# Performance work log

Measured on AMD Instinct MI355X. Metric: run time of the kernel, lower is better.

The kernel has to match this reference:

```python
import jax, jax.numpy as jnp
from jax import lax
import numpy as np

BETA = 0.25
K = 64   # num_embeddings
D = 64   # embedding_dim (must equal K per module's view(-1, D))
HID = 128
RES = 64
N_RES = 2


def _conv(x, w, b=None, stride=1, pad=0):
    y = lax.conv_general_dilated(x, w, (stride, stride), [(pad, pad), (pad, pad)],
                                 dimension_numbers=('NCHW', 'OIHW', 'NCHW'))
    if b is not None:
        y = y + b[None, :, None, None]
    return y


def _deconv(x, w, b, stride, pad):
    # torch ConvTranspose2d weight is (Cin, Cout, k, k); emulate via lhs-dilated conv with flipped kernel
    k = w.shape[2]
    p = k - 1 - pad
    w2 = jnp.transpose(w[:, :, ::-1, ::-1], (1, 0, 2, 3))  # -> (Cout, Cin, k, k)
    y = lax.conv_general_dilated(x, w2, (1, 1), [(p, p), (p, p)], lhs_dilation=(stride, stride),
                                 dimension_numbers=('NCHW', 'OIHW', 'NCHW'))
    return y + b[None, :, None, None]


def _res_block(x, w1, w2):
    # [Residual_Layer]*N_RES shares ONE set of weights; in-place ReLU means skip adds relu(x)
    for _ in range(N_RES):
        r = jax.nn.relu(x)
        h = _conv(r, w1, pad=1)
        h = jax.nn.relu(h)
        h = _conv(h, w2)
        x = r + h
    return jax.nn.relu(x)


def setup_inputs() -> dict:
    key = jax.random.key(0)
    ks = jax.random.split(key, 16)
    f32 = jnp.float32
    s = 0.05
    inp = {
        'x': jax.random.normal(ks[0], (32, 1, 256, 256), f32),
        # encoder
        'enc_c1_w': jax.random.normal(ks[1], (HID // 2, 1, 4, 4), f32) * s,
        'enc_c1_b': jnp.zeros((HID // 2,), f32),
        'enc_c2_w': jax.random.normal(ks[2], (HID, HID // 2, 4, 4), f32) * s,
        'enc_c2_b': jnp.zeros((HID,), f32),
        'enc_c3_w': jax.random.normal(ks[3], (HID, HID, 3, 3), f32) * s,
        'enc_c3_b': jnp.zeros((HID,), f32),
        'enc_r1_w': jax.random.normal(ks[4], (RES, HID, 3, 3), f32) * s,
        'enc_r2_w': jax.random.normal(ks[5], (HID, RES, 1, 1), f32) * s,
        # pre-VQ 1x1 conv: hidden -> K channels
        'vqc_w': jax.random.normal(ks[6], (K, HID, 1, 1), f32) * s,
        'vqc_b': jnp.zeros((K,), f32),
        # codebook, uniform(-1/K, 1/K)
        'emb': jax.random.uniform(ks[7], (K, D), f32, -1.0 / K, 1.0 / K),
        # decoder (ConvTranspose2d weights are (Cin, Cout, k, k))
        'dec_c1_w': jax.random.normal(ks[8], (D, HID, 3, 3), f32) * s,
        'dec_c1_b': jnp.zeros((HID,), f32),
        'dec_r1_w': jax.random.normal(ks[9], (RES, HID, 3, 3), f32) * s,
        'dec_r2_w': jax.random.normal(ks[10], (HID, RES, 1, 1), f32) * s,
        'dec_c2_w': jax.random.normal(ks[11], (HID, HID // 2, 4, 4), f32) * s,
        'dec_c2_b': jnp.zeros((HID // 2,), f32),
        'dec_c3_w': jax.random.normal(ks[12], (HID // 2, 1, 4, 4), f32) * s,
        'dec_c3_b': jnp.zeros((1,), f32),
    }
    return inp


def reference(x, enc_c1_w, enc_c1_b, enc_c2_w, enc_c2_b, enc_c3_w, enc_c3_b,
              enc_r1_w, enc_r2_w, vqc_w, vqc_b, emb,
              dec_c1_w, dec_c1_b, dec_r1_w, dec_r2_w, dec_c2_w, dec_c2_b, dec_c3_w, dec_c3_b):
    # ---- encoder ----
    h = jax.nn.relu(_conv(x, enc_c1_w, enc_c1_b, stride=2, pad=1))
    h = jax.nn.relu(_conv(h, enc_c2_w, enc_c2_b, stride=2, pad=1))
    h = _conv(h, enc_c3_w, enc_c3_b, pad=1)
    h = _res_block(h, enc_r1_w, enc_r2_w)
    z = _conv(h, vqc_w, vqc_b)  # (B, K, 64, 64)

    # ---- VQ ----
    zt = jnp.transpose(z, (0, 2, 3, 1))            # (B, H, W, D)
    flat = zt.reshape(-1, D)                        # (N, D)
    dist = (jnp.sum(flat ** 2, axis=1, keepdims=True)
            + jnp.sum(emb ** 2, axis=1)
            - 2.0 * flat @ emb.T)                   # (N, K)
    idx = jnp.argmin(dist, axis=1)                  # (N,)
    onehot = jax.nn.one_hot(idx, K, dtype=flat.dtype)
    q = (onehot @ emb).reshape(zt.shape)
    commitment = jnp.mean((lax.stop_gradient(q) - zt) ** 2)
    embedding_l = jnp.mean((q - lax.stop_gradient(zt)) ** 2)
    loss = commitment * BETA + embedding_l
    q_st = zt + lax.stop_gradient(q - zt)           # straight-through
    mean_enc = jnp.mean(onehot, axis=0)
    perplexity = jnp.exp(-jnp.sum(mean_enc * jnp.log(mean_enc + 1e-10)))
    qn = jnp.transpose(q_st, (0, 3, 1, 2))          # (B, D, 64, 64)

    # ---- decoder ----
    d = _deconv(qn, dec_c1_w, dec_c1_b, 1, 1)
    d = _res_block(d, dec_r1_w, dec_r2_w)
    d = jax.nn.relu(_deconv(d, dec_c2_w, dec_c2_b, 2, 1))
    x_re = jnp.tanh(_deconv(d, dec_c3_w, dec_c3_b, 2, 1))
    return (loss, x_re, perplexity, qn)
```

## Files before the change

### kernel.cpp

```cpp
#include <hip/hip_runtime.h>
#include <cmath>


static constexpr int NPOS  = 131072;
static constexpr long long NELEM = 8388608;

typedef __attribute__((ext_vector_type(8))) short short8;
typedef __attribute__((ext_vector_type(8))) unsigned short ushort8;
typedef __attribute__((ext_vector_type(4))) float f32x4;

__device__ __forceinline__ unsigned short f2bf(float f) {
  unsigned int x = __float_as_uint(f);
  unsigned int r = (x + 0x7fffu + ((x >> 16) & 1u)) >> 16;
  return (unsigned short)r;
}
__device__ __forceinline__ float bf2f(unsigned short u) {
  return __uint_as_float(((unsigned int)u) << 16);
}
__device__ __forceinline__ void split2(float v, unsigned short& h, unsigned short& l) {
  unsigned short hh = f2bf(v);
  h = hh;
  l = f2bf(v - bf2f(hh));
}

__global__ void __launch_bounds__(256) enc1_t(
    const float* __restrict__ in, const float* __restrict__ w,
    const float* __restrict__ bias,
    unsigned short* __restrict__ outh, unsigned short* __restrict__ outl)
{
  int tid = threadIdx.x;
  int rr = tid >> 7, ox = tid & 127;
  int oy  = blockIdx.x * 2 + rr;
  int oc0 = blockIdx.y * 16;
  int b   = blockIdx.z;

  const float* pl = in + (size_t)b * 65536;
  float v[16];
  #pragma unroll
  for (int ky = 0; ky < 4; ++ky) {
    int iy = 2 * oy - 1 + ky;
    #pragma unroll
    for (int kx = 0; kx < 4; ++kx) {
      int ix = 2 * ox - 1 + kx;
      v[ky * 4 + kx] = (iy >= 0 && iy < 256 && ix >= 0 && ix < 256)
                       ? pl[iy * 256 + ix] : 0.f;
    }
  }
  float acc[16];
  #pragma unroll
  for (int o = 0; o < 16; ++o) acc[o] = bias[oc0 + o];
  #pragma unroll
  for (int t = 0; t < 16; ++t)
    #pragma unroll
    for (int o = 0; o < 16; ++o)
      acc[o] += v[t] * w[(size_t)(oc0 + o) * 16 + t];

  size_t o = ((size_t)b * 16900 + (size_t)(oy + 1) * 130 + (ox + 1)) * 64 + oc0;
  ushort8 h0, h1, l0, l1;
  #pragma unroll
  for (int k = 0; k < 8; ++k) {
    unsigned short hh, ll;
    split2(fmaxf(acc[k], 0.f), hh, ll);      h0[k] = hh; l0[k] = ll;
    split2(fmaxf(acc[k + 8], 0.f), hh, ll);  h1[k] = hh; l1[k] = ll;
  }
  *(ushort8*)(outh + o)     = h0;
  *(ushort8*)(outh + o + 8) = h1;
  *(ushort8*)(outl + o)     = l0;
  *(ushort8*)(outl + o + 8) = l1;
}

template<int IC, int OC, int MODE, bool BIAS, bool RELU>
__global__ void __launch_bounds__(256) mfma_enc(
    const unsigned short* __restrict__ inh, const unsigned short* __restrict__ inl,
    const unsigned short* __restrict__ wh, const unsigned short* __restrict__ wl,
    const float* __restrict__ bias,
    const unsigned short* __restrict__ skh, const unsigned short* __restrict__ skl,
    unsigned short* __restrict__ outh, unsigned short* __restrict__ outl)
{
  constexpr int OM = OC / 16;
  constexpr int NT = (MODE == 0) ? 9 : ((MODE == 1) ? 16 : 1);
  constexpr int IW = (MODE == 1) ? 130 : 66;
  const int in_ss  = IW * IW * IC;
  const int out_ss = 4356 * OC;
  const int tid = threadIdx.x;
  const int wv = tid >> 6, lane = tid & 63;
  const int quad = lane >> 4, l15 = lane & 15;

  const int id = blockIdx.x;
  const int xcd = id & 7;
  const int slot = id >> 3;
  const int bi = slot >> 4;
  const int yb = slot & 15;
  const int b = bi * 8 + xcd;
  const int y = yb * 4 + wv;

  int xs[4];
  #pragma unroll
  for (int j = 0; j < 4; ++j) xs[j] = j * 16 + l15;
  const unsigned short* ibh = inh + (size_t)b * in_ss;
  const unsigned short* ibl = inl + (size_t)b * in_ss;

  f32x4 acc[OM][4];
  #pragma unroll
  for (int m = 0; m < OM; ++m) {
    const int oc0 = m * 16 + quad * 4;
    f32x4 ini = {0.f, 0.f, 0.f, 0.f};
    if (BIAS) {
      float4 bs = *(const float4*)(bias + oc0);
      ini[0] = bs.x; ini[1] = bs.y; ini[2] = bs.z; ini[3] = bs.w;
    }
    #pragma unroll
    for (int j = 0; j < 4; ++j) {
      f32x4 a = ini;
      if (MODE == 2) {
        size_t s = (size_t)b * out_ss + ((size_t)(y + 1) * 66 + (xs[j] + 1)) * OC + oc0;
        ushort4 sh = *(const ushort4*)(skh + s);
        ushort4 sl = *(const ushort4*)(skl + s);
        a[0] += bf2f(sh.x) + bf2f(sl.x);
        a[1] += bf2f(sh.y) + bf2f(sl.y);
        a[2] += bf2f(sh.z) + bf2f(sl.z);
        a[3] += bf2f(sh.w) + bf2f(sl.w);
      }
      acc[m][j] = a;
    }
  }

  for (int t = 0; t < NT; ++t) {
    int off[4];
    #pragma unroll
    for (int j = 0; j < 4; ++j) {
      if (MODE == 1)
        off[j] = ((2 * y + (t >> 2)) * 130 + (2 * xs[j] + (t & 3))) * IC;
      else if (MODE == 0) {
        int dy = t / 3 - 1, dx = t % 3 - 1;
        off[j] = ((y + dy + 1) * 66 + (xs[j] + dx + 1)) * IC;
      } else
        off[j] = ((y + 1) * 66 + (xs[j] + 1)) * IC;
    }
    const unsigned short* wrh = wh + (size_t)t * OC * IC + (size_t)l15 * IC + quad * 8;
    const unsigned short* wrl = wl + (size_t)t * OC * IC + (size_t)l15 * IC + quad * 8;
    #pragma unroll
    for (int k0 = 0; k0 < IC; k0 += 32) {
      short8 bh[4], bl[4];
      #pragma unroll
      for (int j = 0; j < 4; ++j) {
        bh[j] = *(const short8*)(ibh + off[j] + quad * 8 + k0);
        bl[j] = *(const short8*)(ibl + off[j] + quad * 8 + k0);
      }
      #pragma unroll
      for (int m = 0; m < OM; ++m) {
        short8 ah = *(const short8*)(wrh + (size_t)m * 16 * IC + k0);
        short8 al = *(const short8*)(wrl + (size_t)m * 16 * IC + k0);
        #pragma unroll
        for (int j = 0; j < 4; ++j) {
          acc[m][j] = __builtin_amdgcn_mfma_f32_16x16x32_bf16(ah, bh[j], acc[m][j], 0, 0, 0);
          acc[m][j] = __builtin_amdgcn_mfma_f32_16x16x32_bf16(ah, bl[j], acc[m][j], 0, 0, 0);
          acc[m][j] = __builtin_amdgcn_mfma_f32_16x16x32_bf16(al, bh[j], acc[m][j], 0, 0, 0);
        }
      }
    }
  }

  #pragma unroll
  for (int m = 0; m < OM; ++m) {
    const int oc0 = m * 16 + quad * 4;
    #pragma unroll
    for (int j = 0; j < 4; ++j) {
      size_t o = (size_t)b * out_ss + ((size_t)(y + 1) * 66 + (xs[j] + 1)) * OC + oc0;
      ushort4 h4, l4;
      unsigned short hh, ll;
      float v;
      v = acc[m][j][0]; if (RELU) v = fmaxf(v, 0.f); split2(v, hh, ll); h4.x = hh; l4.x = ll;
      v = acc[m][j][1]; if (RELU) v = fmaxf(v, 0.f); split2(v, hh, ll); h4.y = hh; l4.y = ll;
      v = acc[m][j][2]; if (RELU) v = fmaxf(v, 0.f); split2(v, hh, ll); h4.z = hh; l4.z = ll;
      v = acc[m][j][3]; if (RELU) v = fmaxf(v, 0.f); split2(v, hh, ll); h4.w = hh; l4.w = ll;
      *(ushort4*)(outh + o) = h4;
      *(ushort4*)(outl + o) = l4;
    }
  }
}

__global__ void __launch_bounds__(256) vq_mfma(
    const unsigned short* __restrict__ xh, const unsigned short* __restrict__ xl,
    const unsigned short* __restrict__ wvh, const unsigned short* __restrict__ wvl,
    const unsigned short* __restrict__ evh, const unsigned short* __restrict__ evl,
    const float* __restrict__ emb, const float* __restrict__ e2,
    const float* __restrict__ vb,
    float* __restrict__ qn, unsigned short* __restrict__ dqb,
    float* __restrict__ sum_sq, int* __restrict__ hist)
{
  __shared__ float zsh[4][16][65];
  __shared__ int lh[64];
  const int tid = threadIdx.x;
  const int wv = tid >> 6, lane = tid & 63;
  const int quad = lane >> 4, l15 = lane & 15;
  const int y = blockIdx.x;
  const int b = blockIdx.z;
  const int x = wv * 16 + l15;
  if (tid < 64) lh[tid] = 0;

  f32x4 zacc[4];
  #pragma unroll
  for (int m = 0; m < 4; ++m) {
    float4 bv = *(const float4*)(vb + m * 16 + quad * 4);
    zacc[m][0] = bv.x; zacc[m][1] = bv.y; zacc[m][2] = bv.z; zacc[m][3] = bv.w;
  }
  size_t xoff = ((size_t)b * 4356 + (size_t)(y + 1) * 66 + (x + 1)) * 128;
  #pragma unroll
  for (int k0 = 0; k0 < 128; k0 += 32) {
    short8 bh = *(const short8*)(xh + xoff + k0 + quad * 8);
    short8 bl = *(const short8*)(xl + xoff + k0 + quad * 8);
    #pragma unroll
    for (int m = 0; m < 4; ++m) {
      short8 ah = *(const short8*)(wvh + (size_t)(m * 16 + l15) * 128 + k0 + quad * 8);
      short8 al = *(const short8*)(wvl + (size_t)(m * 16 + l15) * 128 + k0 + quad * 8);
      zacc[m] = __builtin_amdgcn_mfma_f32_16x16x32_bf16(ah, bh, zacc[m], 0, 0, 0);
      zacc[m] = __builtin_amdgcn_mfma_f32_16x16x32_bf16(ah, bl, zacc[m], 0, 0, 0);
      zacc[m] = __builtin_amdgcn_mfma_f32_16x16x32_bf16(al, bh, zacc[m], 0, 0, 0);
    }
  }

  float z2p = 0.f;
  #pragma unroll
  for (int m = 0; m < 4; ++m)
    #pragma unroll
    for (int r = 0; r < 4; ++r) {
      float zv = zacc[m][r];
      zsh[wv][l15][m * 16 + quad * 4 + r] = zv;
      z2p += zv * zv;
    }
  z2p += __shfl_xor(z2p, 16);
  z2p += __shfl_xor(z2p, 32);
  __syncthreads();

  f32x4 dacc[4];
  #pragma unroll
  for (int m = 0; m < 4; ++m) { dacc[m][0]=0.f; dacc[m][1]=0.f; dacc[m][2]=0.f; dacc[m][3]=0.f; }
  #pragma unroll
  for (int k0 = 0; k0 < 64; k0 += 32) {
    short8 bh, bl;
    #pragma unroll
    for (int j = 0; j < 8; ++j) {
      float zv = zsh[wv][l15][k0 + quad * 8 + j];
      unsigned short hh, ll;
      split2(zv, hh, ll);
      bh[j] = (short)hh; bl[j] = (short)ll;
    }
    #pragma unroll
    for (int m = 0; m < 4; ++m) {
      short8 ah = *(const short8*)(evh + (size_t)(m * 16 + l15) * 64 + k0 + quad * 8);
      short8 al = *(const short8*)(evl + (size_t)(m * 16 + l15) * 64 + k0 + quad * 8);
      dacc[m] = __builtin_amdgcn_mfma_f32_16x16x32_bf16(ah, bh, dacc[m], 0, 0, 0);
      dacc[m] = __builtin_amdgcn_mfma_f32_16x16x32_bf16(ah, bl, dacc[m], 0, 0, 0);
      dacc[m] = __builtin_amdgcn_mfma_f32_16x16x32_bf16(al, bh, dacc[m], 0, 0, 0);
    }
  }

  float best = INFINITY;
  int bidx = 64;
  #pragma unroll
  for (int m = 0; m < 4; ++m) {
    float4 e2v = *(const float4*)(e2 + m * 16 + quad * 4);
    #pragma unroll
    for (int r = 0; r < 4; ++r) {
      float e2s = (r == 0) ? e2v.x : (r == 1) ? e2v.y : (r == 2) ? e2v.z : e2v.w;
      float d = z2p + e2s - 2.f * dacc[m][r];
      int code = m * 16 + quad * 4 + r;
      if (d < best || (d == best && code < bidx)) { best = d; bidx = code; }
    }
  }
  {
    float ob = __shfl_xor(best, 16);
    int   oi = __shfl_xor(bidx, 16);
    if (ob < best || (ob == best && oi < bidx)) { best = ob; bidx = oi; }
    ob = __shfl_xor(best, 32);
    oi = __shfl_xor(bidx, 32);
    if (ob < best || (ob == best && oi < bidx)) { best = ob; bidx = oi; }
  }

  float ev[16];
  #pragma unroll
  for (int i = 0; i < 4; ++i) {
    float4 t = *(const float4*)(emb + (size_t)bidx * 64 + quad * 16 + i * 4);
    ev[i * 4] = t.x; ev[i * 4 + 1] = t.y; ev[i * 4 + 2] = t.z; ev[i * 4 + 3] = t.w;
  }
  float sq = 0.f;
  #pragma unroll
  for (int i = 0; i < 16; ++i) {
    float zv = zsh[wv][l15][quad * 16 + i];
    float df = ev[i] - zv;
    sq += df * df;
  }
  #pragma unroll
  for (int off = 1; off < 64; off <<= 1) sq += __shfl_xor(sq, off);
  if (lane == 0) atomicAdd(sum_sq, sq);
  if (quad == 0) atomicAdd(&lh[bidx], 1);

  int pos = y * 64 + x;
  float* qb = qn + (size_t)b * 262144 + (size_t)(quad * 16) * 4096 + pos;
  #pragma unroll
  for (int i = 0; i < 16; ++i) qb[(size_t)i * 4096] = ev[i];

  unsigned short* dq = dqb + ((size_t)b * 4356 + (size_t)(y + 1) * 66 + (x + 1)) * 64 + quad * 16;
  ushort8 d0, d1;
  #pragma unroll
  for (int i = 0; i < 8; ++i) { d0[i] = f2bf(ev[i]); d1[i] = f2bf(ev[i + 8]); }
  *(ushort8*)dq = d0;
  *(ushort8*)(dq + 8) = d1;

  __syncthreads();
  if (tid < 64) atomicAdd(&hist[tid], lh[tid]);
}

template<int IC, int OC, int MODE, bool HAS_BIAS, bool HAS_SKIP, bool RELU>
__global__ void __launch_bounds__(256) mfma_conv(
    const unsigned short* __restrict__ in, const unsigned short* __restrict__ wt,
    const float* __restrict__ bias, const unsigned short* __restrict__ skip,
    unsigned short* __restrict__ out, int in_ss, int out_ss)
{
  constexpr int OM = OC / 16;
  constexpr int NT = (MODE == 0) ? 9 : ((MODE == 1) ? 4 : 1);
  constexpr int NP = (MODE == 1) ? 4 : 1;
  constexpr int PERB = 16 * NP;
  const int tid = threadIdx.x;
  const int wv = tid >> 6, lane = tid & 63;
  const int quad = lane >> 4, l15 = lane & 15;

  const int id = blockIdx.x;
  const int xcd = id & 7;
  const int slot = id >> 3;
  const int bi = slot / PERB;
  int r2 = slot - bi * PERB;
  int p = 0;
  if (MODE == 1) { p = r2 >> 4; r2 &= 15; }
  const int yb = r2;
  const int b = bi * 8 + xcd;
  const int y = yb * 4 + wv;

  int ry = 0, rx = 0;
  if (MODE == 1) {
    ry = p >> 1; rx = p & 1;
    wt  += (size_t)p * 4 * OC * IC;
    out += (size_t)p * 4356 * OC;
  }
  int xs[4];
  #pragma unroll
  for (int j = 0; j < 4; ++j) xs[j] = j * 16 + l15;
  const unsigned short* inb = in + (size_t)b * (size_t)in_ss;

  f32x4 acc[OM][4];
  #pragma unroll
  for (int m = 0; m < OM; ++m) {
    const int oc0 = m * 16 + quad * 4;
    f32x4 ini = {0.f, 0.f, 0.f, 0.f};
    if (HAS_BIAS) {
      float4 bs = *(const float4*)(bias + oc0);
      ini[0] = bs.x; ini[1] = bs.y; ini[2] = bs.z; ini[3] = bs.w;
    }
    #pragma unroll
    for (int j = 0; j < 4; ++j) {
      f32x4 a = ini;
      if (HAS_SKIP) {
        size_t s = (size_t)b * (size_t)out_ss + ((size_t)(y + 1) * 66 + (xs[j] + 1)) * OC + oc0;
        ushort4 sv = *(const ushort4*)(skip + s);
        a[0] += bf2f(sv.x); a[1] += bf2f(sv.y); a[2] += bf2f(sv.z); a[3] += bf2f(sv.w);
      }
      acc[m][j] = a;
    }
  }

  #pragma unroll
  for (int t = 0; t < NT; ++t) {
    const int dy = (MODE == 0) ? (t / 3 - 1) : ((MODE == 1) ? (ry - (t >> 1)) : 0);
    const int dx = (MODE == 0) ? (t % 3 - 1) : ((MODE == 1) ? (rx - (t & 1)) : 0);
    const unsigned short* wr = wt + (size_t)t * OC * IC + (size_t)l15 * IC + quad * 8;
    #pragma unroll
    for (int k0 = 0; k0 < IC; k0 += 32) {
      short8 fb[4];
      #pragma unroll
      for (int j = 0; j < 4; ++j)
        fb[j] = *(const short8*)(inb + ((size_t)(y + dy + 1) * 66 + (xs[j] + dx + 1)) * IC + quad * 8 + k0);
      #pragma unroll
      for (int m = 0; m < OM; ++m) {
        short8 fa = *(const short8*)(wr + (size_t)m * 16 * IC + k0);
        #pragma unroll
        for (int j = 0; j < 4; ++j)
          acc[m][j] = __builtin_amdgcn_mfma_f32_16x16x32_bf16(fa, fb[j], acc[m][j], 0, 0, 0);
      }
    }
  }

  #pragma unroll
  for (int m = 0; m < OM; ++m) {
    const int oc0 = m * 16 + quad * 4;
    #pragma unroll
    for (int j = 0; j < 4; ++j) {
      unsigned short* o = out + (size_t)b * (size_t)out_ss
                        + ((size_t)(y + 1) * 66 + (xs[j] + 1)) * OC + oc0;
      ushort4 u4;
      float v;
      v = acc[m][j][0]; if (RELU) v = fmaxf(v, 0.f); u4.x = f2bf(v);
      v = acc[m][j][1]; if (RELU) v = fmaxf(v, 0.f); u4.y = f2bf(v);
      v = acc[m][j][2]; if (RELU) v = fmaxf(v, 0.f); u4.z = f2bf(v);
      v = acc[m][j][3]; if (RELU) v = fmaxf(v, 0.f); u4.w = f2bf(v);
      *(ushort4*)o = u4;
    }
  }
}

__global__ void __launch_bounds__(256) dec3_t(
    const unsigned short* __restrict__ p4, const float* __restrict__ w,
    const float* __restrict__ bias, float* __restrict__ out)
{
  int tid = threadIdx.x;
  int yr = tid >> 7, x = tid & 127;
  int y  = blockIdx.x * 2 + yr;
  int b  = blockIdx.z;

  const int kt[2][2] = {{1, 3}, {0, 2}};
  const int dt[2][2] = {{1, 0}, {2, 1}};

  const unsigned short* base[9];
  #pragma unroll
  for (int dy = 0; dy < 3; ++dy) {
    int iy = y + dy - 1;
    int py = iy & 1, u = iy >> 1;
    #pragma unroll
    for (int dx = 0; dx < 3; ++dx) {
      int ix = x + dx - 1;
      int px = ix & 1, v = ix >> 1;
      base[dy * 3 + dx] = p4 + ((size_t)(b * 4 + py * 2 + px) * 4356
                                + (size_t)(u + 1) * 66 + (v + 1)) * 64;
    }
  }

  float acc[4] = {0.f, 0.f, 0.f, 0.f};
  for (int oct = 0; oct < 8; ++oct) {
    ushort8 s[9];
    #pragma unroll
    for (int t = 0; t < 9; ++t)
      s[t] = *(const ushort8*)(base[t] + oct * 8);

    #pragma unroll
    for (int j = 0; j < 8; ++j) {
      const float* wp = w + (size_t)(oct * 8 + j) * 16;
      float v9[9];
      #pragma unroll
      for (int t = 0; t < 9; ++t) v9[t] = bf2f(s[t][j]);
      #pragma unroll
      for (int ry = 0; ry < 2; ++ry)
        #pragma unroll
        for (int rx = 0; rx < 2; ++rx)
          #pragma unroll
          for (int a = 0; a < 2; ++a)
            #pragma unroll
            for (int c2 = 0; c2 < 2; ++c2)
              acc[ry * 2 + rx] += v9[dt[ry][a] * 3 + dt[rx][c2]]
                                * wp[kt[ry][a] * 4 + kt[rx][c2]];
    }
  }

  float b0 = bias[0];
  float* ob = out + (size_t)b * 65536;
  #pragma unroll
  for (int ry = 0; ry < 2; ++ry)
    #pragma unroll
    for (int rx = 0; rx < 2; ++rx)
      ob[(2 * y + ry) * 256 + 2 * x + rx] = tanhf(acc[ry * 2 + rx] + b0);
}

struct RingArgs {
  unsigned short* p[5];
  int icl[5];
  int H[5];
  int planes[5];
};
__global__ void rings_k(RingArgs a)
{
  int bi = blockIdx.y;
  if ((int)blockIdx.x >= a.planes[bi]) return;
  int H = a.H[bi];
  int icl = a.icl[bi];
  int C = 1 << icl;
  unsigned short* pl = a.p[bi] + (size_t)blockIdx.x * H * H * C;
  int cells = 4 * H - 4;
  int total = cells * C;
  for (int idx = threadIdx.x; idx < total; idx += 256) {
    int cell = idx >> icl;
    int e = idx & (C - 1);
    int row, col;
    if (cell < H)             { row = 0;     col = cell; }
    else if (cell < 2 * H)    { row = H - 1; col = cell - H; }
    else if (cell < 2 * H + (H - 2)) { row = cell - 2 * H + 1; col = 0; }
    else                      { row = cell - 2 * H - (H - 2) + 1; col = H - 1; }
    pl[((size_t)row * H + col) * C + e] = 0;
  }
}

__global__ void repack_k(const float* __restrict__ c1w, const float* __restrict__ r1w,
                         const float* __restrict__ r2w, const float* __restrict__ c2w,
                         unsigned short* __restrict__ W)
{
  int idx = blockIdx.x * 256 + threadIdx.x;
  if (idx >= 286720) return;
  float val;
  if (idx < 73728) {
    int t = idx / 8192, rem = idx & 8191;
    int oc = rem >> 6, ic = rem & 63;
    int ky = t / 3, kx = t - ky * 3;
    val = c1w[((ic * 128 + oc) * 3 + (2 - ky)) * 3 + (2 - kx)];
  } else if (idx < 147456) {
    int j = idx - 73728;
    int t = j / 8192, rem = j & 8191;
    int oc = rem >> 7, ic = rem & 127;
    int ky = t / 3, kx = t - ky * 3;
    val = r1w[((oc * 128 + ic) * 3 + ky) * 3 + kx];
  } else if (idx < 155648) {
    int j = idx - 147456;
    int oc = j >> 6, ic = j & 63;
    val = r2w[oc * 64 + ic];
  } else {
    int j = idx - 155648;
    int p = j >> 15;
    int t2 = (j >> 13) & 3;
    int oc = (j >> 7) & 63;
    int ic = j & 127;
    int ry = p >> 1, rx = p & 1;
    int aY = t2 >> 1, aX = t2 & 1;
    int ky = aY ? (3 - ry) : (1 - ry);
    int kx = aX ? (3 - rx) : (1 - rx);
    val = c2w[((ic * 64 + oc) * 4 + ky) * 4 + kx];
  }
  W[idx] = f2bf(val);
}

__global__ void repack_enc_k(const float* __restrict__ c2w, const float* __restrict__ c3w,
                             const float* __restrict__ r1w, const float* __restrict__ r2w,
                             unsigned short* __restrict__ Wh, unsigned short* __restrict__ Wl)
{
  int idx = blockIdx.x * 256 + threadIdx.x;
  if (idx >= 360448) return;
  float val;
  if (idx < 131072) {
    int t = idx >> 13;
    int rem = idx & 8191;
    int oc = rem >> 6, ic = rem & 63;
    val = c2w[(((size_t)oc * 64 + ic) << 4) + t];
  } else if (idx < 278528) {
    int j = idx - 131072;
    int t = j / 16384;
    int rem = j & 16383;
    int oc = rem >> 7, ic = rem & 127;
    val = c3w[((size_t)oc * 128 + ic) * 9 + t];
  } else if (idx < 352256) {
    int j = idx - 278528;
    int t = j / 8192;
    int rem = j & 8191;
    int oc = rem >> 7, ic = rem & 127;
    val = r1w[((size_t)oc * 128 + ic) * 9 + t];
  } else {
    int j = idx - 352256;
    int oc = j >> 6, ic = j & 63;
    val = r2w[oc * 64 + ic];
  }
  unsigned short h = f2bf(val);
  Wh[idx] = h;
  Wl[idx] = f2bf(val - bf2f(h));
}

__global__ void repack_vq_k(const float* __restrict__ vqw, const float* __restrict__ emb,
                            unsigned short* __restrict__ wvh, unsigned short* __restrict__ wvl,
                            unsigned short* __restrict__ evh, unsigned short* __restrict__ evl,
                            float* __restrict__ e2)
{
  int idx = blockIdx.x * 256 + threadIdx.x;
  if (idx < 8192) {
    float v = vqw[idx];
    unsigned short h = f2bf(v);
    wvh[idx] = h;
    wvl[idx] = f2bf(v - bf2f(h));
  } else if (idx < 12288) {
    int j = idx - 8192;
    float v = emb[j];
    unsigned short h = f2bf(v);
    evh[j] = h;
    evl[j] = f2bf(v - bf2f(h));
  }
  if (idx < 64) {
    float s = 0.f;
    for (int d = 0; d < 64; ++d) { float e = emb[idx * 64 + d]; s += e * e; }
    e2[idx] = s;
  }
}

__global__ void init_k(float* sum_sq, int* hist)
{
  int t = threadIdx.x;
  if (t == 0) sum_sq[0] = 0.f;
  if (t < 64) hist[t] = 0;
}

__global__ void finalize_k(const float* __restrict__ sum_sq, const int* __restrict__ hist,
                           float* __restrict__ loss_out, float* __restrict__ perp_out)
{
  if (threadIdx.x == 0) {
    float mse = sum_sq[0] / (float)NELEM;
    loss_out[0] = 1.25f * mse;
    float ent = 0.f;
    for (int k = 0; k < 64; ++k) {
      float p = (float)hist[k] / (float)NPOS;
      ent += p * logf(p + 1e-10f);
    }
    perp_out[0] = expf(-ent);
  }
}

extern "C" void kernel_launch(void* const* d_in, const int* in_sizes, int n_in,
                              void* d_out, int out_size, void* d_ws, size_t ws_size,
                              hipStream_t stream)
{
  const float* x        = (const float*)d_in[0];
  const float* enc_c1_w = (const float*)d_in[1];
  const float* enc_c1_b = (const float*)d_in[2];
  const float* enc_c2_w = (const float*)d_in[3];
  const float* enc_c2_b = (const float*)d_in[4];
  const float* enc_c3_w = (const float*)d_in[5];
  const float* enc_c3_b = (const float*)d_in[6];
  const float* enc_r1_w = (const float*)d_in[7];
  const float* enc_r2_w = (const float*)d_in[8];
  const float* vqc_w    = (const float*)d_in[9];
  const float* vqc_b    = (const float*)d_in[10];
  const float* emb      = (const float*)d_in[11];
  const float* dec_c1_w = (const float*)d_in[12];
  const float* dec_c1_b = (const float*)d_in[13];
  const float* dec_r1_w = (const float*)d_in[14];
  const float* dec_r2_w = (const float*)d_in[15];
  const float* dec_c2_w = (const float*)d_in[16];
  const float* dec_c2_b = (const float*)d_in[17];
  const float* dec_c3_w = (const float*)d_in[18];
  const float* dec_c3_b = (const float*)d_in[19];

  float* out      = (float*)d_out;
  float* loss_out = out;
  float* xre_out  = out + 1;
  float* perp_out = out + 1 + 2097152;
  float* qn_out   = out + 2 + 2097152;

  float* sum_sq = (float*)d_ws;
  int*   hist   = (int*)d_ws + 1;
  char*  pool   = (char*)d_ws + 1024;

  unsigned short* Wd  = (unsigned short*)(pool + 0);
  unsigned short* Weh = (unsigned short*)(pool + 600000);
  unsigned short* Wel = (unsigned short*)(pool + 1400000);
  unsigned short* Wvh = (unsigned short*)(pool + 2121728);
  unsigned short* Wvl = (unsigned short*)(pool + 2138112);
  unsigned short* Evh = (unsigned short*)(pool + 2154496);
  unsigned short* Evl = (unsigned short*)(pool + 2162688);
  float*          E2  = (float*)(pool + 2170880);
  unsigned short* E1h = (unsigned short*)(pool + 2200000);
  unsigned short* E1l = (unsigned short*)(pool + 71500000);
  unsigned short* B2h = (unsigned short*)(pool + 141000000);
  unsigned short* B2l = (unsigned short*)(pool + 177000000);
  unsigned short* R0h = (unsigned short*)(pool + 2200000);
  unsigned short* R0l = (unsigned short*)(pool + 38000000);
  unsigned short* Hh  = (unsigned short*)(pool + 74000000);
  unsigned short* Hl  = (unsigned short*)(pool + 92000000);
  unsigned short* X1h = (unsigned short*)(pool + 141000000);
  unsigned short* X1l = (unsigned short*)(pool + 177000000);
  unsigned short* X2h = (unsigned short*)(pool + 2200000);
  unsigned short* X2l = (unsigned short*)(pool + 38000000);
  unsigned short* Dq  = (unsigned short*)(pool + 213000000);
  unsigned short* Y1  = (unsigned short*)(pool + 141000000);
  unsigned short* S   = (unsigned short*)(pool + 110000000);
  unsigned short* Y2  = (unsigned short*)(pool + 177000000);
  unsigned short* P4  = (unsigned short*)(pool + 2200000);

  const int SS64  = 278784;
  const int SS128 = 557568;
  const int SSP4  = 1115136;

  hipLaunchKernelGGL(init_k, dim3(1), dim3(128), 0, stream, sum_sq, hist);
  hipLaunchKernelGGL(repack_k, dim3(1120), dim3(256), 0, stream,
                     dec_c1_w, dec_r1_w, dec_r2_w, dec_c2_w, Wd);
  hipLaunchKernelGGL(repack_enc_k, dim3(1408), dim3(256), 0, stream,
                     enc_c2_w, enc_c3_w, enc_r1_w, enc_r2_w, Weh, Wel);
  hipLaunchKernelGGL(repack_vq_k, dim3(48), dim3(256), 0, stream,
                     vqc_w, emb, Wvh, Wvl, Evh, Evl, E2);

  {
    RingArgs a;
    a.p[0] = E1h; a.icl[0] = 6; a.H[0] = 130; a.planes[0] = 32;
    a.p[1] = E1l; a.icl[1] = 6; a.H[1] = 130; a.planes[1] = 32;
    a.p[2] = B2h; a.icl[2] = 7; a.H[2] = 66;  a.planes[2] = 32;
    a.p[3] = B2l; a.icl[3] = 7; a.H[3] = 66;  a.planes[3] = 32;
    a.p[4] = Dq;  a.icl[4] = 6; a.H[4] = 66;  a.planes[4] = 32;
    hipLaunchKernelGGL(rings_k, dim3(32, 5), dim3(256), 0, stream, a);
  }

  hipLaunchKernelGGL(enc1_t, dim3(64, 4, 32), dim3(256), 0, stream,
                     x, enc_c1_w, enc_c1_b, E1h, E1l);
  hipLaunchKernelGGL((mfma_enc<64, 128, 1, true, true>),
                     dim3(512), dim3(256), 0, stream,
                     E1h, E1l, Weh, Wel, enc_c2_b, nullptr, nullptr, B2h, B2l);

  {
    RingArgs a;
    a.p[0] = R0h; a.icl[0] = 7; a.H[0] = 66; a.planes[0] = 32;
    a.p[1] = R0l; a.icl[1] = 7; a.H[1] = 66; a.planes[1] = 32;
    a.p[2] = Hh;  a.icl[2] = 6; a.H[2] = 66; a.planes[2] = 32;
    a.p[3] = Hl;  a.icl[3] = 6; a.H[3] = 66; a.planes[3] = 32;
    a.p[4] = S;   a.icl[4] = 6; a.H[4] = 66; a.planes[4] = 32;
    hipLaunchKernelGGL(rings_k, dim3(32, 5), dim3(256), 0, stream, a);
  }

  hipLaunchKernelGGL((mfma_enc<128, 128, 0, true, true>),
                     dim3(512), dim3(256), 0, stream,
                     B2h, B2l, Weh + 131072, Wel + 131072, enc_c3_b,
                     nullptr, nullptr, R0h, R0l);

  {
    RingArgs a;
    a.p[0] = X1h; a.icl[0] = 7; a.H[0] = 66; a.planes[0] = 32;
    a.p[1] = X1l; a.icl[1] = 7; a.H[1] = 66; a.planes[1] = 32;
    a.p[2] = nullptr; a.icl[2] = 0; a.H[2] = 2; a.planes[2] = 0;
    a.p[3] = nullptr; a.icl[3] = 0; a.H[3] = 2; a.planes[3] = 0;
    a.p[4] = nullptr; a.icl[4] = 0; a.H[4] = 2; a.planes[4] = 0;
    hipLaunchKernelGGL(rings_k, dim3(32, 2), dim3(256), 0, stream, a);
  }

  hipLaunchKernelGGL((mfma_enc<128, 64, 0, false, true>),
                     dim3(512), dim3(256), 0, stream,
                     R0h, R0l, Weh + 278528, Wel + 278528, nullptr,
                     nullptr, nullptr, Hh, Hl);
  hipLaunchKernelGGL((mfma_enc<64, 128, 2, false, true>),
                     dim3(512), dim3(256), 0, stream,
                     Hh, Hl, Weh + 352256, Wel + 352256, nullptr,
                     R0h, R0l, X1h, X1l);

  {
    RingArgs a;
    a.p[0] = X2h; a.icl[0] = 7; a.H[0] = 66; a.planes[0] = 32;
    a.p[1] = X2l; a.icl[1] = 7; a.H[1] = 66; a.planes[1] = 32;
    a.p[2] = nullptr; a.icl[2] = 0; a.H[2] = 2; a.planes[2] = 0;
    a.p[3] = nullptr; a.icl[3] = 0; a.H[3] = 2; a.planes[3] = 0;
    a.p[4] = nullptr; a.icl[4] = 0; a.H[4] = 2; a.planes[4] = 0;
    hipLaunchKernelGGL(rings_k, dim3(32, 2), dim3(256), 0, stream, a);
  }

  hipLaunchKernelGGL((mfma_enc<128, 64, 0, false, true>),
                     dim3(512), dim3(256), 0, stream,
                     X1h, X1l, Weh + 278528, Wel + 278528, nullptr,
                     nullptr, nullptr, Hh, Hl);
  hipLaunchKernelGGL((mfma_enc<64, 128, 2, false, true>),
                     dim3(512), dim3(256), 0, stream,
                     Hh, Hl, Weh + 352256, Wel + 352256, nullptr,
                     X1h, X1l, X2h, X2l);

  hipLaunchKernelGGL(vq_mfma, dim3(64, 1, 32), dim3(256), 0, stream,
                     X2h, X2l, Wvh, Wvl, Evh, Evl, emb, E2, vqc_b,
                     qn_out, Dq, sum_sq, hist);

  {
    RingArgs a;
    a.p[0] = Y1;  a.icl[0] = 7; a.H[0] = 66; a.planes[0] = 32;
    a.p[1] = Y2;  a.icl[1] = 7; a.H[1] = 66; a.planes[1] = 32;
    a.p[2] = P4;  a.icl[2] = 6; a.H[2] = 66; a.planes[2] = 128;
    a.p[3] = nullptr; a.icl[3] = 0; a.H[3] = 2; a.planes[3] = 0;
    a.p[4] = nullptr; a.icl[4] = 0; a.H[4] = 2; a.planes[4] = 0;
    hipLaunchKernelGGL(rings_k, dim3(128, 3), dim3(256), 0, stream, a);
  }

  hipLaunchKernelGGL((mfma_conv<64, 128, 0, true, false, true>),
                     dim3(512), dim3(256), 0, stream,
                     Dq, Wd, dec_c1_b, nullptr, Y1, SS64, SS128);
  hipLaunchKernelGGL((mfma_conv<128, 64, 0, false, false, true>),
                     dim3(512), dim3(256), 0, stream,
                     Y1, Wd + 73728, nullptr, nullptr, S, SS128, SS64);
  hipLaunchKernelGGL((mfma_conv<64, 128, 2, false, true, true>),
                     dim3(512), dim3(256), 0, stream,
                     S, Wd + 147456, nullptr, Y1, Y2, SS64, SS128);
  hipLaunchKernelGGL((mfma_conv<128, 64, 0, false, false, true>),
                     dim3(512), dim3(256), 0, stream,
                     Y2, Wd + 73728, nullptr, nullptr, S, SS128, SS64);
  hipLaunchKernelGGL((mfma_conv<64, 128, 2, false, true, true>),
                     dim3(512), dim3(256), 0, stream,
                     S, Wd + 147456, nullptr, Y2, Y1, SS64, SS128);

  hipLaunchKernelGGL((mfma_conv<128, 64, 1, true, false, true>),
                     dim3(2048), dim3(256), 0, stream,
                     Y1, Wd + 155648, dec_c2_b, nullptr, P4, SS128, SSP4);

  hipLaunchKernelGGL(dec3_t, dim3(64, 1, 32), dim3(256), 0, stream,
                     P4, dec_c3_w, dec_c3_b, xre_out);

  hipLaunchKernelGGL(finalize_k, dim3(1), dim3(64), 0, stream,
                     sum_sq, hist, loss_out, perp_out);
}
```

Before: 1.858 ms.

## Stage 3x3 conv input tiles in LDS for encoder and decoder MFMA kernels

Adds new 3x3 conv kernels (split-bf16 encoder and plain-bf16 decoder variants) that cooperatively load a 6-row by 66-column halo tile of 32 input channels into padded shared memory. All nine taps then read from LDS instead of issuing repeated global loads. Dispatch for every 3x3 conv in the encoder and decoder is switched to these kernels, and the now-unused MODE 0 paths are removed from the generic kernels. The aim is to cut redundant global and L2 traffic from overlapping taps, at the cost of LDS use, lower occupancy and two barriers per channel chunk.

```diff
diff --git a/kernel.cpp b/kernel.cpp
--- a/kernel.cpp
+++ b/kernel.cpp
@@ -67,6 +67,201 @@
   *(ushort8*)(outh + o + 8) = h1;
   *(ushort8*)(outl + o)     = l0;
   *(ushort8*)(outl + o + 8) = l1;
+}
+
+template<int IC, int OC, bool BIAS, bool RELU>
+__global__ void __launch_bounds__(256) mfma_enc3(
+    const unsigned short* __restrict__ inh, const unsigned short* __restrict__ inl,
+    const unsigned short* __restrict__ wh, const unsigned short* __restrict__ wl,
+    const float* __restrict__ bias,
+    unsigned short* __restrict__ outh, unsigned short* __restrict__ outl)
+{
+  constexpr int OM = OC / 16;
+  constexpr int CP = 36;
+  __shared__ unsigned short sh[6 * 66 * CP];
+  __shared__ unsigned short sl[6 * 66 * CP];
+  const int in_ss  = 4356 * IC;
+  const int out_ss = 4356 * OC;
+  const int tid = threadIdx.x;
+  const int wv = tid >> 6, lane = tid & 63;
+  const int quad = lane >> 4, l15 = lane & 15;
+
+  const int id = blockIdx.x;
+  const int xcd = id & 7;
+  const int slot = id >> 3;
+  const int bi = slot >> 4;
+  const int yb = slot & 15;
+  const int b = bi * 8 + xcd;
+  const int y0 = yb * 4;
+  const int y = y0 + wv;
+
+  int xs[4];
+  #pragma unroll
+  for (int j = 0; j < 4; ++j) xs[j] = j * 16 + l15;
+  const unsigned short* ibh = inh + (size_t)b * in_ss;
+  const unsigned short* ibl = inl + (size_t)b * in_ss;
+
+  f32x4 acc[OM][4];
+  #pragma unroll
+  for (int m = 0; m < OM; ++m) {
+    const int oc0 = m * 16 + quad * 4;
+    f32x4 ini = {0.f, 0.f, 0.f, 0.f};
+    if (BIAS) {
+      float4 bs = *(const float4*)(bias + oc0);
+      ini[0] = bs.x; ini[1] = bs.y; ini[2] = bs.z; ini[3] = bs.w;
+    }
+    #pragma unroll
+    for (int j = 0; j < 4; ++j) acc[m][j] = ini;
+  }
+
+  for (int k0 = 0; k0 < IC; k0 += 32) {
+    for (int idx = tid; idx < 1584; idx += 256) {
+      int row = idx / 264;
+      int rem = idx - row * 264;
+      int col = rem >> 2;
+      int v = (rem & 3) << 3;
+      size_t g = ((size_t)(y0 + row) * 66 + col) * IC + k0 + v;
+      int s = (row * 66 + col) * CP + v;
+      *(ushort8*)&sh[s] = *(const ushort8*)(ibh + g);
+      *(ushort8*)&sl[s] = *(const ushort8*)(ibl + g);
+    }
+    __syncthreads();
+
+    #pragma unroll
+    for (int t = 0; t < 9; ++t) {
+      const int dy = t / 3 - 1, dx = t % 3 - 1;
+      short8 bh4[4], bl4[4];
+      #pragma unroll
+      for (int j = 0; j < 4; ++j) {
+        int s = ((wv + dy + 1) * 66 + xs[j] + dx + 1) * CP + quad * 8;
+        bh4[j] = *(const short8*)&sh[s];
+        bl4[j] = *(const short8*)&sl[s];
+      }
+      const unsigned short* wrh = wh + (size_t)t * OC * IC + (size_t)l15 * IC + quad * 8 + k0;
+      const unsigned short* wrl = wl + (size_t)t * OC * IC + (size_t)l15 * IC + quad * 8 + k0;
+      #pragma unroll
+      for (int m = 0; m < OM; ++m) {
+        short8 ah = *(const short8*)(wrh + (size_t)m * 16 * IC);
+        short8 al = *(const short8*)(wrl + (size_t)m * 16 * IC);
+        #pragma unroll
+        for (int j = 0; j < 4; ++j) {
+          acc[m][j] = __builtin_amdgcn_mfma_f32_16x16x32_bf16(ah, bh4[j], acc[m][j], 0, 0, 0);
+          acc[m][j] = __builtin_amdgcn_mfma_f32_16x16x32_bf16(ah, bl4[j], acc[m][j], 0, 0, 0);
+          acc[m][j] = __builtin_amdgcn_mfma_f32_16x16x32_bf16(al, bh4[j], acc[m][j], 0, 0, 0);
+        }
+      }
+    }
+    __syncthreads();
+  }
+
+  #pragma unroll
+  for (int m = 0; m < OM; ++m) {
+    const int oc0 = m * 16 + quad * 4;
+    #pragma unroll
+    for (int j = 0; j < 4; ++j) {
+      size_t o = (size_t)b * out_ss + ((size_t)(y + 1) * 66 + (xs[j] + 1)) * OC + oc0;
+      ushort4 h4, l4;
+      unsigned short hh, ll;
+      float v;
+      v = acc[m][j][0]; if (RELU) v = fmaxf(v, 0.f); split2(v, hh, ll); h4.x = hh; l4.x = ll;
+      v = acc[m][j][1]; if (RELU) v = fmaxf(v, 0.f); split2(v, hh, ll); h4.y = hh; l4.y = ll;
+      v = acc[m][j][2]; if (RELU) v = fmaxf(v, 0.f); split2(v, hh, ll); h4.z = hh; l4.z = ll;
+      v = acc[m][j][3]; if (RELU) v = fmaxf(v, 0.f); split2(v, hh, ll); h4.w = hh; l4.w = ll;
+      *(ushort4*)(outh + o) = h4;
+      *(ushort4*)(outl + o) = l4;
+    }
+  }
+}
+
+template<int IC, int OC, bool HAS_BIAS, bool RELU>
+__global__ void __launch_bounds__(256) mfma_dec3(
+    const unsigned short* __restrict__ in, const unsigned short* __restrict__ wt,
+    const float* __restrict__ bias, unsigned short* __restrict__ out)
+{
+  constexpr int OM = OC / 16;
+  constexpr int CP = 36;
+  __shared__ unsigned short sp[6 * 66 * CP];
+  const int in_ss  = 4356 * IC;
+  const int out_ss = 4356 * OC;
+  const int tid = threadIdx.x;
+  const int wv = tid >> 6, lane = tid & 63;
+  const int quad = lane >> 4, l15 = lane & 15;
+
+  const int id = blockIdx.x;
+  const int xcd = id & 7;
+  const int slot = id >> 3;
+  const int bi = slot >> 4;
+  const int yb = slot & 15;
+  const int b = bi * 8 + xcd;
+  const int y0 = yb * 4;
+  const int y = y0 + wv;
+
+  int xs[4];
+  #pragma unroll
+  for (int j = 0; j < 4; ++j) xs[j] = j * 16 + l15;
+  const unsigned short* inb = in + (size_t)b * in_ss;
+
+  f32x4 acc[OM][4];
+  #pragma unroll
+  for (int m = 0; m < OM; ++m) {
+    const int oc0 = m * 16 + quad * 4;
+    f32x4 ini = {0.f, 0.f, 0.f, 0.f};
+    if (HAS_BIAS) {
+      float4 bs = *(const float4*)(bias + oc0);
+      ini[0] = bs.x; ini[1] = bs.y; ini[2] = bs.z; ini[3] = bs.w;
+    }
+    #pragma unroll
+    for (int j = 0; j < 4; ++j) acc[m][j] = ini;
+  }
+
+  for (int k0 = 0; k0 < IC; k0 += 32) {
+    for (int idx = tid; idx < 1584; idx += 256) {
+      int row = idx / 264;
+      int rem = idx - row * 264;
+      int col = rem >> 2;
+      int v = (rem & 3) << 3;
+      size_t g = ((size_t)(y0 + row) * 66 + col) * IC + k0 + v;
+      *(ushort8*)&sp[(row * 66 + col) * CP + v] = *(const ushort8*)(inb + g);
+    }
+    __syncthreads();
+
+    #pragma unroll
+    for (int t = 0; t < 9; ++t) {
+      const int dy = t / 3 - 1, dx = t % 3 - 1;
+      short8 fb[4];
+      #pragma unroll
+      for (int j = 0; j < 4; ++j) {
+        int s = ((wv + dy + 1) * 66 + xs[j] + dx + 1) * CP + quad * 8;
+        fb[j] = *(const short8*)&sp[s];
+      }
+      const unsigned short* wr = wt + (size_t)t * OC * IC + (size_t)l15 * IC + quad * 8 + k0;
+      #pragma unroll
+      for (int m = 0; m < OM; ++m) {
+        short8 fa = *(const short8*)(wr + (size_t)m * 16 * IC);
+        #pragma unroll
+        for (int j = 0; j < 4; ++j)
+          acc[m][j] = __builtin_amdgcn_mfma_f32_16x16x32_bf16(fa, fb[j], acc[m][j], 0, 0, 0);
+      }
+    }
+    __syncthreads();
+  }
+
+  #pragma unroll
+  for (int m = 0; m < OM; ++m) {
+    const int oc0 = m * 16 + quad * 4;
+    #pragma unroll
+    for (int j = 0; j < 4; ++j) {
+      unsigned short* o = out + (size_t)b * out_ss
+                        + ((size_t)(y + 1) * 66 + (xs[j] + 1)) * OC + oc0;
+      ushort4 u4;
+      float v;
+      v = acc[m][j][0]; if (RELU) v = fmaxf(v, 0.f); u4.x = f2bf(v);
+      v = acc[m][j][1]; if (RELU) v = fmaxf(v, 0.f); u4.y = f2bf(v);
+      v = acc[m][j][2]; if (RELU) v = fmaxf(v, 0.f); u4.z = f2bf(v);
+      v = acc[m][j][3]; if (RELU) v = fmaxf(v, 0.f); u4.w = f2bf(v);
+      *(ushort4*)o = u4;
+    }
+  }
 }
 
 template<int IC, int OC, int MODE, bool BIAS, bool RELU>
@@ -131,10 +326,7 @@
     for (int j = 0; j < 4; ++j) {
       if (MODE == 1)
         off[j] = ((2 * y + (t >> 2)) * 130 + (2 * xs[j] + (t & 3))) * IC;
-      else if (MODE == 0) {
-        int dy = t / 3 - 1, dx = t % 3 - 1;
-        off[j] = ((y + dy + 1) * 66 + (xs[j] + dx + 1)) * IC;
-      } else
+      else
         off[j] = ((y + 1) * 66 + (xs[j] + 1)) * IC;
     }
     const unsigned short* wrh = wh + (size_t)t * OC * IC + (size_t)l15 * IC + quad * 8;
@@ -319,7 +511,7 @@
     unsigned short* __restrict__ out, int in_ss, int out_ss)
 {
   constexpr int OM = OC / 16;
-  constexpr int NT = (MODE == 0) ? 9 : ((MODE == 1) ? 4 : 1);
+  constexpr int NT = (MODE == 1) ? 4 : 1;
   constexpr int NP = (MODE == 1) ? 4 : 1;
   constexpr int PERB = 16 * NP;
   const int tid = threadIdx.x;
@@ -371,8 +563,8 @@
 
   #pragma unroll
   for (int t = 0; t < NT; ++t) {
-    const int dy = (MODE == 0) ? (t / 3 - 1) : ((MODE == 1) ? (ry - (t >> 1)) : 0);
-    const int dx = (MODE == 0) ? (t % 3 - 1) : ((MODE == 1) ? (rx - (t & 1)) : 0);
+    const int dy = (MODE == 1) ? (ry - (t >> 1)) : 0;
+    const int dx = (MODE == 1) ? (rx - (t & 1)) : 0;
     const unsigned short* wr = wt + (size_t)t * OC * IC + (size_t)l15 * IC + quad * 8;
     #pragma unroll
     for (int k0 = 0; k0 < IC; k0 += 32) {
@@ -714,10 +906,9 @@
     hipLaunchKernelGGL(rings_k, dim3(32, 5), dim3(256), 0, stream, a);
   }
 
-  hipLaunchKernelGGL((mfma_enc<128, 128, 0, true, true>),
-                     dim3(512), dim3(256), 0, stream,
-                     B2h, B2l, Weh + 131072, Wel + 131072, enc_c3_b,
-                     nullptr, nullptr, R0h, R0l);
+  hipLaunchKernelGGL((mfma_enc3<128, 128, true, true>),
+                     dim3(512), dim3(256), 0, stream,
+                     B2h, B2l, Weh + 131072, Wel + 131072, enc_c3_b, R0h, R0l);
 
   {
     RingArgs a;
@@ -729,10 +920,9 @@
     hipLaunchKernelGGL(rings_k, dim3(32, 2), dim3(256), 0, stream, a);
   }
 
-  hipLaunchKernelGGL((mfma_enc<128, 64, 0, false, true>),
-                     dim3(512), dim3(256), 0, stream,
-                     R0h, R0l, Weh + 278528, Wel + 278528, nullptr,
-                     nullptr, nullptr, Hh, Hl);
+  hipLaunchKernelGGL((mfma_enc3<128, 64, false, true>),
+                     dim3(512), dim3(256), 0, stream,
+                     R0h, R0l, Weh + 278528, Wel + 278528, nullptr, Hh, Hl);
   hipLaunchKernelGGL((mfma_enc<64, 128, 2, false, true>),
                      dim3(512), dim3(256), 0, stream,
                      Hh, Hl, Weh + 352256, Wel + 352256, nullptr,
@@ -748,10 +938,9 @@
     hipLaunchKernelGGL(rings_k, dim3(32, 2), dim3(256), 0, stream, a);
   }
 
-  hipLaunchKernelGGL((mfma_enc<128, 64, 0, false, true>),
-                     dim3(512), dim3(256), 0, stream,
-                     X1h, X1l, Weh + 278528, Wel + 278528, nullptr,
-                     nullptr, nullptr, Hh, Hl);
+  hipLaunchKernelGGL((mfma_enc3<128, 64, false, true>),
+                     dim3(512), dim3(256), 0, stream,
+                     X1h, X1l, Weh + 278528, Wel + 278528, nullptr, Hh, Hl);
   hipLaunchKernelGGL((mfma_enc<64, 128, 2, false, true>),
                      dim3(512), dim3(256), 0, stream,
                      Hh, Hl, Weh + 352256, Wel + 352256, nullptr,
@@ -771,18 +960,18 @@
     hipLaunchKernelGGL(rings_k, dim3(128, 3), dim3(256), 0, stream, a);
   }
 
-  hipLaunchKernelGGL((mfma_conv<64, 128, 0, true, false, true>),
-                     dim3(512), dim3(256), 0, stream,
-                     Dq, Wd, dec_c1_b, nullptr, Y1, SS64, SS128);
-  hipLaunchKernelGGL((mfma_conv<128, 64, 0, false, false, true>),
-                     dim3(512), dim3(256), 0, stream,
-                     Y1, Wd + 73728, nullptr, nullptr, S, SS128, SS64);
+  hipLaunchKernelGGL((mfma_dec3<64, 128, true, true>),
+                     dim3(512), dim3(256), 0, stream,
+                     Dq, Wd, dec_c1_b, Y1);
+  hipLaunchKernelGGL((mfma_dec3<128, 64, false, true>),
+                     dim3(512), dim3(256), 0, stream,
+                     Y1, Wd + 73728, nullptr, S);
   hipLaunchKernelGGL((mfma_conv<64, 128, 2, false, true, true>),
                      dim3(512), dim3(256), 0, stream,
                      S, Wd + 147456, nullptr, Y1, Y2, SS64, SS128);
-  hipLaunchKernelGGL((mfma_conv<128, 64, 0, false, false, true>),
-                     dim3(512), dim3(256), 0, stream,
-                     Y2, Wd + 73728, nullptr, nullptr, S, SS128, SS64);
+  hipLaunchKernelGGL((mfma_dec3<128, 64, false, true>),
+                     dim3(512), dim3(256), 0, stream,
+                     Y2, Wd + 73728, nullptr, S);
   hipLaunchKernelGGL((mfma_conv<64, 128, 2, false, true, true>),
                      dim3(512), dim3(256), 0, stream,
                      S, Wd + 147456, nullptr, Y2, Y1, SS64, SS128);
```

After: 1.696 ms. 1.1x faster.
